# Kernel optimization log

Hardware: AMD Instinct MI355X
Metric: run time of the kernel (lower is better)

The kernel has to match this reference:

```python
import jax, jax.numpy as jnp
import numpy as np

N = 100000      # n_nodes
D = 128         # n_features
H = 64          # n_filters (hidden)
C = 40          # n_classes
NNZ = 3200000   # n_edges (avg degree 32)


def setup_inputs() -> dict:
    key = jax.random.key(0)
    ks = jax.random.split(key, 6)
    x = jax.random.normal(ks[0], (N, D), dtype=jnp.float32)
    edge_idx = jax.random.randint(ks[1], (2, NNZ), 0, N, dtype=jnp.int32)
    edge_weight = jnp.ones((NNZ,), dtype=jnp.float32)
    # Glorot-ish init for linear weights
    W1 = jax.random.normal(ks[2], (D, H), dtype=jnp.float32) / np.sqrt(D)
    b1 = jnp.zeros((H,), dtype=jnp.float32)
    W2 = jax.random.normal(ks[3], (H, C), dtype=jnp.float32) / np.sqrt(H)
    b2 = jnp.zeros((C,), dtype=jnp.float32)
    return {"x": x, "edge_idx": edge_idx, "edge_weight": edge_weight,
            "W1": W1, "b1": b1, "W2": W2, "b2": b2}


def gcn_norm(edge_idx, edge_weight, n):
    """PyG gcn_norm: add self-loops (weight 1), symmetric D^-1/2 A D^-1/2."""
    loop = jnp.arange(n, dtype=edge_idx.dtype)
    row = jnp.concatenate([edge_idx[0], loop])  # source
    col = jnp.concatenate([edge_idx[1], loop])  # target
    w = jnp.concatenate([edge_weight, jnp.ones((n,), edge_weight.dtype)])
    deg = jax.ops.segment_sum(w, col, num_segments=n)
    dis = jnp.where(deg > 0, jax.lax.rsqrt(deg), 0.0)
    norm = dis[row] * w * dis[col]
    return row, col, norm


def gcn_conv(h, row, col, norm, W, b):
    # linear transform then sparse aggregation: out[col] += norm * (h @ W)[row]
    h = h @ W
    out = jax.ops.segment_sum(h[row] * norm[:, None], col, num_segments=h.shape[0])
    return out + b


def reference(x, edge_idx, edge_weight, W1, b1, W2, b2):
    n = x.shape[0]
    # adjacency normalized once and cached (do_normalize_adj_once=True)
    row, col, norm = gcn_norm(edge_idx, edge_weight, n)
    h = gcn_conv(x, row, col, norm, W1, b1)
    h = jax.nn.relu(h)
    # dropout is identity at inference time
    out = gcn_conv(h, row, col, norm, W2, b2)
    return out
```

## Files before the change

### kernel.cpp

```cpp
#include <hip/hip_runtime.h>
#include <hip/hip_bf16.h>
#include <cstdint>

#define NN   100000
#define DD   128
#define HH   64
#define CC   40
#define NNZE 3200000


__global__ void k_zero(int* cnt, int n) {
    int i = blockIdx.x * blockDim.x + threadIdx.x;
    if (i < n) cnt[i] = 0;
}

__global__ void k_count(const int* __restrict__ col, int* cnt, int* rank, int nnz) {
    int e = blockIdx.x * blockDim.x + threadIdx.x;
    if (e < nnz) rank[e] = atomicAdd(&cnt[col[e]], 1);
}


__global__ void scan_k1(const int* __restrict__ cnt, int* offs, int* bsum, int n) {
    __shared__ int s[256];
    int t = threadIdx.x, b = blockIdx.x;
    int base = b * 1024 + t * 4;
    int v0 = (base + 0 < n) ? cnt[base + 0] : 0;
    int v1 = (base + 1 < n) ? cnt[base + 1] : 0;
    int v2 = (base + 2 < n) ? cnt[base + 2] : 0;
    int v3 = (base + 3 < n) ? cnt[base + 3] : 0;
    int tsum = v0 + v1 + v2 + v3;
    s[t] = tsum;
    __syncthreads();
    for (int off = 1; off < 256; off <<= 1) {
        int x = (t >= off) ? s[t - off] : 0;
        __syncthreads();
        s[t] += x;
        __syncthreads();
    }
    int incl = s[t];
    int p = incl - tsum;
    if (base + 0 < n) offs[base + 0] = p; p += v0;
    if (base + 1 < n) offs[base + 1] = p; p += v1;
    if (base + 2 < n) offs[base + 2] = p; p += v2;
    if (base + 3 < n) offs[base + 3] = p;
    if (t == 255) bsum[b] = incl;
}

__global__ void scan_k2(int* bsum, int nb, int* offs, int n) {
    if (threadIdx.x == 0 && blockIdx.x == 0) {
        int run = 0;
        for (int i = 0; i < nb; i++) { int v = bsum[i]; bsum[i] = run; run += v; }
        offs[n] = run;
    }
}

__global__ void scan_k3(int* offs, const int* __restrict__ bsum, int n) {
    int i = blockIdx.x * blockDim.x + threadIdx.x;
    if (i < n) offs[i] += bsum[i >> 10];
}


__global__ void k_fill(const int* __restrict__ row, const int* __restrict__ col,
                       const float* __restrict__ w, const int* __restrict__ rank,
                       const int* __restrict__ offs,
                       int* csr_src, float* csr_a, int nnz) {
    int e = blockIdx.x * blockDim.x + threadIdx.x;
    if (e < nnz) {
        int pos = offs[col[e]] + rank[e];
        csr_src[pos] = row[e];
        csr_a[pos] = w[e];
    }
}


__global__ void k_degdis(const int* __restrict__ offs, const float* __restrict__ csr_a,
                         float* dis, int n) {
    int i = blockIdx.x * blockDim.x + threadIdx.x;
    if (i < n) {
        float s = 1.0f;
        int e0 = offs[i], e1 = offs[i + 1];
        for (int j = e0; j < e1; j++) s += csr_a[j];
        dis[i] = s > 0.f ? rsqrtf(s) : 0.f;
    }
}


__global__ void k_scale(float* csr_a, const int* __restrict__ csr_src,
                        const float* __restrict__ dis, int nnz) {
    int i = blockIdx.x * blockDim.x + threadIdx.x;
    if (i < nnz) csr_a[i] *= dis[csr_src[i]];
}


__global__ __launch_bounds__(256) void k_gemm1(const float* __restrict__ x,
                                               const float* __restrict__ W1,
                                               float* __restrict__ h1, int n) {
    __shared__ float ws[128 * 64];
    __shared__ float xs[16 * 129];
    int t = threadIdx.x;
    for (int i = t; i < 128 * 64; i += 256) ws[i] = W1[i];
    int row0 = blockIdx.x * 64;
    int r = t >> 4, cg = t & 15;
    for (int p = 0; p < 4; p++) {
        __syncthreads();
        int rbase = row0 + p * 16;
        for (int i = t; i < 512; i += 256) {
            int li = i * 4;
            int rr = li >> 7, kk = li & 127;
            float4 v = make_float4(0.f, 0.f, 0.f, 0.f);
            if (rbase + rr < n) v = *(const float4*)&x[(rbase + rr) * 128 + kk];
            xs[rr * 129 + kk + 0] = v.x;
            xs[rr * 129 + kk + 1] = v.y;
            xs[rr * 129 + kk + 2] = v.z;
            xs[rr * 129 + kk + 3] = v.w;
        }
        __syncthreads();
        float4 acc = make_float4(0.f, 0.f, 0.f, 0.f);
        for (int k = 0; k < 128; k++) {
            float xa = xs[r * 129 + k];
            float4 w4 = *(const float4*)&ws[k * 64 + cg * 4];
            acc.x += xa * w4.x; acc.y += xa * w4.y;
            acc.z += xa * w4.z; acc.w += xa * w4.w;
        }
        int rowi = rbase + r;
        if (rowi < n) *(float4*)&h1[rowi * 64 + cg * 4] = acc;
    }
}


__global__ __launch_bounds__(256) void k_agg1(const float* __restrict__ h1,
                                              const int* __restrict__ offs,
                                              const int* __restrict__ csr_src,
                                              const float* __restrict__ csr_a,
                                              const float* __restrict__ dis,
                                              const float* __restrict__ b1,
                                              const float* __restrict__ W2,
                                              float* __restrict__ g, int n) {
    __shared__ float w2s[64 * 40];
    __shared__ float sh2[4][64];
    __shared__ int   ssrc[4][64];
    __shared__ float sa[4][64];
    int t = threadIdx.x;
    for (int i = t; i < 64 * 40; i += 256) w2s[i] = W2[i];
    __syncthreads();
    int w = t >> 6, l = t & 63;
    int c = blockIdx.x * 4 + w;
    if (c >= n) return;
    float dc = dis[c];
    float selfh = h1[c * 64 + l];
    float acc = 0.f;
    int start = offs[c], end = offs[c + 1];
    for (int base = start; base < end; base += 64) {
        int m = end - base; if (m > 64) m = 64;
        if (l < m) { ssrc[w][l] = csr_src[base + l]; sa[w][l] = csr_a[base + l]; }
        for (int j = 0; j < m; j++) {
            acc += sa[w][j] * h1[ssrc[w][j] * 64 + l];
        }
    }
    float hv = dc * acc + dc * dc * selfh + b1[l];
    hv = hv > 0.f ? hv : 0.f;
    sh2[w][l] = hv;
    if (l < 40) {
        float gv = 0.f;
        for (int k = 0; k < 64; k++) gv += sh2[w][k] * w2s[k * 40 + l];
        g[c * 40 + l] = gv;
    }
}


__global__ __launch_bounds__(256) void k_agg2(const float* __restrict__ g,
                                              const int* __restrict__ offs,
                                              const int* __restrict__ csr_src,
                                              const float* __restrict__ csr_a,
                                              const float* __restrict__ dis,
                                              const float* __restrict__ b2,
                                              float* __restrict__ out, int n) {
    __shared__ int   ssrc[4][64];
    __shared__ float sa[4][64];
    int t = threadIdx.x;
    int w = t >> 6, l = t & 63;
    int c = blockIdx.x * 4 + w;
    if (c >= n) return;
    float dc = dis[c];
    float acc = 0.f;
    int start = offs[c], end = offs[c + 1];
    for (int base = start; base < end; base += 64) {
        int m = end - base; if (m > 64) m = 64;
        if (l < m) { ssrc[w][l] = csr_src[base + l]; sa[w][l] = csr_a[base + l]; }
        if (l < 40) {
            for (int j = 0; j < m; j++) {
                acc += sa[w][j] * g[ssrc[w][j] * 40 + l];
            }
        }
    }
    if (l < 40) {
        float selfg = g[c * 40 + l];
        out[c * 40 + l] = dc * acc + dc * dc * selfg + b2[l];
    }
}


extern "C" void kernel_launch(void* const* d_in, const int* in_sizes, int n_in,
                              void* d_out, int out_size, void* d_ws, size_t ws_size,
                              hipStream_t stream) {
    const float* x  = (const float*)d_in[0];
    const int*   ei = (const int*)d_in[1];
    const float* ew = (const float*)d_in[2];
    const float* W1 = (const float*)d_in[3];
    const float* b1 = (const float*)d_in[4];
    const float* W2 = (const float*)d_in[5];
    const float* b2 = (const float*)d_in[6];
    float* out = (float*)d_out;

    const int n = NN, nnz = NNZE;
    const int* erow = ei;
    const int* ecol = ei + nnz;

    char* p = (char*)d_ws;
    auto alloc = [&](size_t bytes) {
        void* r = (void*)p;
        p += (bytes + 255) & ~(size_t)255;
        return r;
    };
    float* dis     = (float*)alloc((size_t)n * 4);
    int*   offs    = (int*)  alloc((size_t)(n + 1) * 4);
    int*   cnt     = (int*)  alloc((size_t)n * 4);
    int*   bsum    = (int*)  alloc((size_t)128 * 4);
    int*   csr_src = (int*)  alloc((size_t)nnz * 4);
    float* csr_a   = (float*)alloc((size_t)nnz * 4);
    float* h1      = (float*)alloc((size_t)n * HH * 4);
    float* g       = (float*)alloc((size_t)n * CC * 4);
    int*   rank    = (int*)h1;
    (void)ws_size;

    const int NB_N   = (n + 255) / 256;
    const int NB_E   = (nnz + 255) / 256;
    const int NB_SC  = (n + 1023) / 1024;

    k_zero  <<<NB_N, 256, 0, stream>>>(cnt, n);
    k_count <<<NB_E, 256, 0, stream>>>(ecol, cnt, rank, nnz);
    scan_k1 <<<NB_SC, 256, 0, stream>>>(cnt, offs, bsum, n);
    scan_k2 <<<1, 64, 0, stream>>>(bsum, NB_SC, offs, n);
    scan_k3 <<<NB_N, 256, 0, stream>>>(offs, bsum, n);
    k_fill  <<<NB_E, 256, 0, stream>>>(erow, ecol, ew, rank, offs, csr_src, csr_a, nnz);
    k_degdis<<<NB_N, 256, 0, stream>>>(offs, csr_a, dis, n);
    k_scale <<<NB_E, 256, 0, stream>>>(csr_a, csr_src, dis, nnz);
    k_gemm1 <<<(n + 63) / 64, 256, 0, stream>>>(x, W1, h1, n);
    k_agg1  <<<(n + 3) / 4, 256, 0, stream>>>(h1, offs, csr_src, csr_a, dis, b1, W2, g, n);
    k_agg2  <<<(n + 3) / 4, 256, 0, stream>>>(g, offs, csr_src, csr_a, dis, b2, out, n);
}
```

Measured before the change: 696.4 us.

## Pack CSR source and weight into int2, vectorize edge passes, fold scaling into aggregation

```diff
diff --git a/kernel.cpp b/kernel.cpp
--- a/kernel.cpp
+++ b/kernel.cpp
@@ -14,9 +14,16 @@
     if (i < n) cnt[i] = 0;
 }
 
-__global__ void k_count(const int* __restrict__ col, int* cnt, int* rank, int nnz) {
-    int e = blockIdx.x * blockDim.x + threadIdx.x;
-    if (e < nnz) rank[e] = atomicAdd(&cnt[col[e]], 1);
+__global__ void k_count(const int* __restrict__ col, int* cnt, int* rank, int nnz4) {
+    int i = blockIdx.x * blockDim.x + threadIdx.x;
+    if (i < nnz4) {
+        int4 c = ((const int4*)col)[i];
+        int r0 = atomicAdd(&cnt[c.x], 1);
+        int r1 = atomicAdd(&cnt[c.y], 1);
+        int r2 = atomicAdd(&cnt[c.z], 1);
+        int r3 = atomicAdd(&cnt[c.w], 1);
+        ((int4*)rank)[i] = make_int4(r0, r1, r2, r3);
+    }
 }
 
 
@@ -63,32 +70,30 @@
 __global__ void k_fill(const int* __restrict__ row, const int* __restrict__ col,
                        const float* __restrict__ w, const int* __restrict__ rank,
                        const int* __restrict__ offs,
-                       int* csr_src, float* csr_a, int nnz) {
-    int e = blockIdx.x * blockDim.x + threadIdx.x;
-    if (e < nnz) {
-        int pos = offs[col[e]] + rank[e];
-        csr_src[pos] = row[e];
-        csr_a[pos] = w[e];
-    }
-}
-
-
-__global__ void k_degdis(const int* __restrict__ offs, const float* __restrict__ csr_a,
+                       int2* __restrict__ csr, int nnz4) {
+    int i = blockIdx.x * blockDim.x + threadIdx.x;
+    if (i < nnz4) {
+        int4   r  = ((const int4*)row)[i];
+        int4   c  = ((const int4*)col)[i];
+        int4   rk = ((const int4*)rank)[i];
+        float4 wv = ((const float4*)w)[i];
+        csr[offs[c.x] + rk.x] = make_int2(r.x, __float_as_int(wv.x));
+        csr[offs[c.y] + rk.y] = make_int2(r.y, __float_as_int(wv.y));
+        csr[offs[c.z] + rk.z] = make_int2(r.z, __float_as_int(wv.z));
+        csr[offs[c.w] + rk.w] = make_int2(r.w, __float_as_int(wv.w));
+    }
+}
+
+
+__global__ void k_degdis(const int* __restrict__ offs, const int2* __restrict__ csr,
                          float* dis, int n) {
     int i = blockIdx.x * blockDim.x + threadIdx.x;
     if (i < n) {
         float s = 1.0f;
         int e0 = offs[i], e1 = offs[i + 1];
-        for (int j = e0; j < e1; j++) s += csr_a[j];
+        for (int j = e0; j < e1; j++) s += __int_as_float(csr[j].y);
         dis[i] = s > 0.f ? rsqrtf(s) : 0.f;
     }
-}
-
-
-__global__ void k_scale(float* csr_a, const int* __restrict__ csr_src,
-                        const float* __restrict__ dis, int nnz) {
-    int i = blockIdx.x * blockDim.x + threadIdx.x;
-    if (i < nnz) csr_a[i] *= dis[csr_src[i]];
 }
 
 
@@ -130,8 +135,7 @@
 
 __global__ __launch_bounds__(256) void k_agg1(const float* __restrict__ h1,
                                               const int* __restrict__ offs,
-                                              const int* __restrict__ csr_src,
-                                              const float* __restrict__ csr_a,
+                                              const int2* __restrict__ csr,
                                               const float* __restrict__ dis,
                                               const float* __restrict__ b1,
                                               const float* __restrict__ W2,
@@ -152,7 +156,11 @@
     int start = offs[c], end = offs[c + 1];
     for (int base = start; base < end; base += 64) {
         int m = end - base; if (m > 64) m = 64;
-        if (l < m) { ssrc[w][l] = csr_src[base + l]; sa[w][l] = csr_a[base + l]; }
+        if (l < m) {
+            int2 pk = csr[base + l];
+            ssrc[w][l] = pk.x;
+            sa[w][l] = __int_as_float(pk.y) * dis[pk.x];
+        }
         for (int j = 0; j < m; j++) {
             acc += sa[w][j] * h1[ssrc[w][j] * 64 + l];
         }
@@ -170,8 +178,7 @@
 
 __global__ __launch_bounds__(256) void k_agg2(const float* __restrict__ g,
                                               const int* __restrict__ offs,
-                                              const int* __restrict__ csr_src,
-                                              const float* __restrict__ csr_a,
+                                              const int2* __restrict__ csr,
                                               const float* __restrict__ dis,
                                               const float* __restrict__ b2,
                                               float* __restrict__ out, int n) {
@@ -186,7 +193,11 @@
     int start = offs[c], end = offs[c + 1];
     for (int base = start; base < end; base += 64) {
         int m = end - base; if (m > 64) m = 64;
-        if (l < m) { ssrc[w][l] = csr_src[base + l]; sa[w][l] = csr_a[base + l]; }
+        if (l < m) {
+            int2 pk = csr[base + l];
+            ssrc[w][l] = pk.x;
+            sa[w][l] = __int_as_float(pk.y) * dis[pk.x];
+        }
         if (l < 40) {
             for (int j = 0; j < m; j++) {
                 acc += sa[w][j] * g[ssrc[w][j] * 40 + l];
@@ -222,30 +233,28 @@
         p += (bytes + 255) & ~(size_t)255;
         return r;
     };
-    float* dis     = (float*)alloc((size_t)n * 4);
-    int*   offs    = (int*)  alloc((size_t)(n + 1) * 4);
-    int*   cnt     = (int*)  alloc((size_t)n * 4);
-    int*   bsum    = (int*)  alloc((size_t)128 * 4);
-    int*   csr_src = (int*)  alloc((size_t)nnz * 4);
-    float* csr_a   = (float*)alloc((size_t)nnz * 4);
-    float* h1      = (float*)alloc((size_t)n * HH * 4);
-    float* g       = (float*)alloc((size_t)n * CC * 4);
-    int*   rank    = (int*)h1;
+    float* dis  = (float*)alloc((size_t)n * 4);
+    int*   offs = (int*)  alloc((size_t)(n + 1) * 4);
+    int*   cnt  = (int*)  alloc((size_t)n * 4);
+    int*   bsum = (int*)  alloc((size_t)128 * 4);
+    int2*  csr  = (int2*) alloc((size_t)nnz * 8);
+    float* h1   = (float*)alloc((size_t)n * HH * 4);
+    float* g    = (float*)alloc((size_t)n * CC * 4);
+    int*   rank = (int*)h1;
     (void)ws_size;
 
-    const int NB_N   = (n + 255) / 256;
-    const int NB_E   = (nnz + 255) / 256;
-    const int NB_SC  = (n + 1023) / 1024;
+    const int NB_N  = (n + 255) / 256;
+    const int NB_E4 = (nnz / 4 + 255) / 256;
+    const int NB_SC = (n + 1023) / 1024;
 
     k_zero  <<<NB_N, 256, 0, stream>>>(cnt, n);
-    k_count <<<NB_E, 256, 0, stream>>>(ecol, cnt, rank, nnz);
+    k_count <<<NB_E4, 256, 0, stream>>>(ecol, cnt, rank, nnz / 4);
     scan_k1 <<<NB_SC, 256, 0, stream>>>(cnt, offs, bsum, n);
     scan_k2 <<<1, 64, 0, stream>>>(bsum, NB_SC, offs, n);
     scan_k3 <<<NB_N, 256, 0, stream>>>(offs, bsum, n);
-    k_fill  <<<NB_E, 256, 0, stream>>>(erow, ecol, ew, rank, offs, csr_src, csr_a, nnz);
-    k_degdis<<<NB_N, 256, 0, stream>>>(offs, csr_a, dis, n);
-    k_scale <<<NB_E, 256, 0, stream>>>(csr_a, csr_src, dis, nnz);
+    k_fill  <<<NB_E4, 256, 0, stream>>>(erow, ecol, ew, rank, offs, csr, nnz / 4);
+    k_degdis<<<NB_N, 256, 0, stream>>>(offs, csr, dis, n);
     k_gemm1 <<<(n + 63) / 64, 256, 0, stream>>>(x, W1, h1, n);
-    k_agg1  <<<(n + 3) / 4, 256, 0, stream>>>(h1, offs, csr_src, csr_a, dis, b1, W2, g, n);
-    k_agg2  <<<(n + 3) / 4, 256, 0, stream>>>(g, offs, csr_src, csr_a, dis, b2, out, n);
-}
+    k_agg1  <<<(n + 3) / 4, 256, 0, stream>>>(h1, offs, csr, dis, b1, W2, g, n);
+    k_agg2  <<<(n + 3) / 4, 256, 0, stream>>>(g, offs, csr, dis, b2, out, n);
+}
```

New measurement: 629.9 us. 9.6% less time.
